# Kernel optimization log

Hardware: AMD Instinct MI355X
Metric: run time of the kernel (lower is better)

The kernel has to match this reference:

```python
import jax, jax.numpy as jnp
import numpy as np

P, M, N, H, B, E, K = 50, 512, 1024, 256, 8, 400, 5
ALPHA_MAX, TAU_MAX, RHO_MAX, ETA_MAX = 0.01, 1.0, 1.0, 1.0
LEAK = 0.01  # F.leaky_relu default slope


def _lrelu(x):
    return jnp.where(x >= 0, x, LEAK * x)


def _layernorm(x, g, b, eps=1e-5):
    mu = jnp.mean(x, axis=-1, keepdims=True)
    var = jnp.mean((x - mu) ** 2, axis=-1, keepdims=True)
    return (x - mu) * jax.lax.rsqrt(var + eps) * g + b


def setup_inputs() -> dict:
    ks = iter(jax.random.split(jax.random.key(0), 16))

    def w(fin, fout):
        return jax.random.normal(next(ks), (fin, fout), jnp.float32) * np.float32(np.sqrt(2.0 / (fin + fout)))

    H4 = 4 * H
    inp = {
        'A': jax.random.normal(next(ks), (1, P, M, N), jnp.float32) * 0.05,
        'b': jax.random.normal(next(ks), (B, P, M, 1), jnp.float32),
        'W1': w(2 * N, H), 'b1': jnp.zeros(H), 'bn1_s': jnp.ones(H), 'bn1_t': jnp.zeros(H),
        'W2': w(H, 2 * H), 'b2': jnp.zeros(2 * H), 'bn2_s': jnp.ones(2 * H), 'bn2_t': jnp.zeros(2 * H),
        'W3': w(2 * H, H4), 'b3': jnp.zeros(H4), 'bn3_s': jnp.ones(H4), 'bn3_t': jnp.zeros(H4),
        'W4': w(H4, H4), 'b4': jnp.zeros(H4), 'bn4_s': jnp.ones(H4), 'bn4_t': jnp.zeros(H4),
        'W5': w(H4, H4), 'b5': jnp.zeros(H4), 'bn5_s': jnp.ones(H4), 'bn5_t': jnp.zeros(H4),
        'ln_g': jnp.ones(H4), 'ln_b': jnp.zeros(H4),
        'Wd1': w(P * H4, H4), 'bd1': jnp.zeros(H4), 'lnd1_g': jnp.ones(H4), 'lnd1_b': jnp.zeros(H4),
        'Wd2': w(H4, 2 * H), 'bd2': jnp.zeros(2 * H), 'lnd2_g': jnp.ones(2 * H), 'lnd2_b': jnp.zeros(2 * H),
        'Wd3': w(2 * H, H), 'bd3': jnp.zeros(H), 'lnd3_g': jnp.ones(H), 'lnd3_b': jnp.zeros(H),
        'Wfc': w(H, 4) * 0.1, 'bfc': jnp.zeros(4),
        'edge_index': jax.random.randint(next(ks), (2, E), 0, P),
    }
    return inp


def reference(A, b, W1, b1, bn1_s, bn1_t, W2, b2, bn2_s, bn2_t, W3, b3, bn3_s, bn3_t,
              W4, b4, bn4_s, bn4_t, W5, b5, bn5_s, bn5_t, ln_g, ln_b,
              Wd1, bd1, lnd1_g, lnd1_b, Wd2, bd2, lnd2_g, lnd2_b, Wd3, bd3, lnd3_g, lnd3_b,
              Wfc, bfc, edge_index):
    A0 = A[0]                                             # [P,M,N]
    AtA = jnp.einsum('pmi,pmj->pij', A0, A0)              # [P,N,N]  (compute_Atx(A))
    Atb = jnp.einsum('pmn,bpm->bpn', A0, b[..., 0])[..., None]  # [B,P,N,1]

    src, dst = edge_index[0], edge_index[1]
    ones_e = jnp.ones((E,), A.dtype)
    # sum_neighbors: out-degree of each node p, shape broadcastable to [B,P,1,1]
    sum_nb = jax.ops.segment_sum(ones_e, src, num_segments=P)[None, :, None, None]

    # GCNConv normalization with self loops: norm_ij = deg_i^-1/2 * deg_j^-1/2
    sl = jnp.arange(P)
    src_a = jnp.concatenate([src, sl])
    dst_a = jnp.concatenate([dst, sl])
    deg = jax.ops.segment_sum(jnp.ones((E + P,), A.dtype), dst_a, num_segments=P)
    dinv = jax.lax.rsqrt(deg)
    coef = (dinv[src_a] * dinv[dst_a])[:, None]           # [E+P,1]

    convs = [(W1, b1, bn1_s, bn1_t), (W2, b2, bn2_s, bn2_t), (W3, b3, bn3_s, bn3_t),
             (W4, b4, bn4_s, bn4_t), (W5, b5, bn5_s, bn5_t)]

    def gconv(x, W, bias):                                # x: [P,Cin]
        xw = x @ W
        return jax.ops.segment_sum(xw[src_a] * coef, dst_a, num_segments=P) + bias

    def encode_one(feat):                                 # feat: [P,2N]
        x = feat
        for (W, bias, s, t) in convs:
            # leaky_relu -> BatchNorm1d (eval: affine scale/shift) -> dropout (eval: id)
            x = _lrelu(gconv(x, W, bias)) * s + t
        return _layernorm(x, ln_g, ln_b).reshape(-1)      # [P*4H]

    enc = jax.vmap(encode_one)

    y = jnp.zeros((B, P, N, 1), A.dtype)
    U = jnp.zeros_like(y)
    delta = jnp.zeros_like(y)
    Ys = []
    for k in range(K):
        AtAy = jnp.einsum('pij,bpj->bpi', AtA, y[..., 0])[..., None]  # [B,P,N,1]
        feat = jnp.concatenate([AtAy, Atb], axis=2)[..., 0]           # [B,P,2N]
        code = enc(feat)                                              # [B,P*4H]
        h = _lrelu(_layernorm(code @ Wd1 + bd1, lnd1_g, lnd1_b))
        h = _lrelu(_layernorm(h @ Wd2 + bd2, lnd2_g, lnd2_b))
        h = _lrelu(_layernorm(h @ Wd3 + bd3, lnd3_g, lnd3_b))
        hyp = jnp.clip(jax.nn.sigmoid(h @ Wfc + bfc), 1e-4, 0.99).reshape(B, 4, 1, 1, 1)
        alpha = hyp[:, 0] * ALPHA_MAX
        tau = hyp[:, 1] * TAU_MAX
        rho = hyp[:, 2] * RHO_MAX
        eta = hyp[:, 3] * ETA_MAX
        g = AtAy - Atb + jnp.sign(y) * tau + U * sum_nb + delta * rho
        mg = max(30.0, 100.0 - k)
        g = jnp.clip(g, -mg, mg)
        mv = max(10.0, 200.0 - k * 3)
        y = jnp.clip(y - alpha * g, -mv, mv)
        # compute_delta: for each directed edge (s,d): delta[s]+= (y_s-y_d); delta[d]-= (y_s-y_d)
        diff = y[:, src] - y[:, dst]                                  # [B,E,N,1]
        delta = jnp.zeros_like(y).at[:, src].add(diff).at[:, dst].add(-diff)
        U = jnp.clip(U + delta * eta, -mv, mv)
        Ys.append(y)
    return jnp.stack(Ys)                                              # [K,B,P,N,1]
```

## Files before the change

### kernel.cpp

```cpp
#include <hip/hip_runtime.h>

#define PP 50
#define MM 512
#define NN 1024

constexpr size_t F_ATB   = 0;
constexpr size_t F_ATAY  = F_ATB   + 409600;
constexpr size_t F_Y     = F_ATAY  + 409600;
constexpr size_t F_U     = F_Y     + 409600;
constexpr size_t F_DELTA = F_U     + 409600;
constexpr size_t F_BT    = F_DELTA + 409600;
constexpr size_t F_AYT   = F_BT    + 204800;
constexpr size_t F_Z     = F_AYT   + 204800;
constexpr size_t F_X0    = F_Z     + 917504;
constexpr size_t F_X1    = F_X0    + 409600;
constexpr size_t F_CODET = F_X1    + 409600;
constexpr size_t F_PART  = F_CODET + 409600;
constexpr size_t F_DPART = F_PART  + 3670016;
constexpr size_t F_DPART2= F_DPART + 2097152;
constexpr size_t F_H1    = F_DPART2+ 32768;
constexpr size_t F_H2    = F_H1    + 8192;
constexpr size_t F_H3    = F_H2    + 4096;
constexpr size_t F_HYP   = F_H3    + 2048;
constexpr size_t F_GCCO  = F_HYP   + 64;
constexpr size_t F_SUMNB = F_GCCO  + 512;
constexpr size_t F_END   = F_SUMNB + 64;

__device__ __forceinline__ float lrelu(float v) { return v >= 0.f ? v : 0.01f * v; }

__device__ __forceinline__ void bred2(float& s1, float& s2, float* sm) {
  #pragma unroll
  for (int off = 32; off > 0; off >>= 1) {
    s1 += __shfl_down(s1, off);
    s2 += __shfl_down(s2, off);
  }
  int w = threadIdx.x >> 6, l = threadIdx.x & 63;
  if (l == 0) { sm[w] = s1; sm[4 + w] = s2; }
  __syncthreads();
  s1 = sm[0] + sm[1] + sm[2] + sm[3];
  s2 = sm[4] + sm[5] + sm[6] + sm[7];
}

__global__ __launch_bounds__(512) void ksetup(const int* __restrict__ ei, float* sumnb,
                                              float* gccoef, int* gcoff, int* gcsrc,
                                              int* nbroff, int* nbridx) {
  __shared__ int cin[PP];
  __shared__ int cou[PP];
  __shared__ float sdinv[PP];
  __shared__ int goff[PP + 1], noff[PP + 1];
  int t = threadIdx.x;
  const int* src = ei;
  const int* dst = ei + 400;
  if (t < PP) { cin[t] = 0; cou[t] = 0; }
  __syncthreads();
  if (t < 400) {
    atomicAdd(&cou[src[t]], 1);
    atomicAdd(&cin[dst[t]], 1);
  }
  __syncthreads();
  if (t < PP) {
    sdinv[t] = rsqrtf((float)(cin[t] + 1));
    sumnb[t] = (float)cou[t];
  }
  __syncthreads();
  if (t == 0) {
    goff[0] = 0; noff[0] = 0;
    for (int p = 0; p < PP; ++p) {
      goff[p + 1] = goff[p] + cin[p] + 1;
      noff[p + 1] = noff[p] + cin[p] + cou[p];
    }
  }
  __syncthreads();
  if (t <= PP) { gcoff[t] = goff[t]; nbroff[t] = noff[t]; }
  if (t < 400) {
    int d = dst[t], s = src[t];
    int slot = 0;
    for (int e = 0; e < t; ++e) slot += (dst[e] == d) ? 1 : 0;
    int pos = goff[d] + slot;
    gcsrc[pos] = s;
    gccoef[pos] = sdinv[s] * sdinv[d];
  }
  if (t < PP) {
    int pos = goff[t] + cin[t];
    gcsrc[pos] = t;
    gccoef[pos] = sdinv[t] * sdinv[t];
  }
  if (t < 400) {
    int s = src[t], d = dst[t];
    int so = 0, si = 0;
    for (int e = 0; e < t; ++e) {
      so += (src[e] == s) ? 1 : 0;
      si += (dst[e] == d) ? 1 : 0;
    }
    nbridx[noff[s] + so] = d;
    nbridx[noff[d] + cou[d] + si] = s;
  }
}

__global__ __launch_bounds__(256) void kbt(const float* __restrict__ b, float* __restrict__ bt) {
  int i = blockIdx.x * 256 + threadIdx.x;
  int bb = i / (PP * MM);
  int r = i - bb * (PP * MM);
  bt[r * 8 + bb] = b[i];
}

__global__ __launch_bounds__(256) void katz(const float* __restrict__ A, const float* __restrict__ q,
                                            float* __restrict__ outv) {
  __shared__ float red[4][64][8];
  int nb = blockIdx.x, p = blockIdx.y, t = threadIdx.x;
  int ln = t & 63, mg = t >> 6;
  int n = nb * 64 + ln;
  float acc[8] = {0, 0, 0, 0, 0, 0, 0, 0};
  const float* ap = A + ((size_t)p * MM + mg * 128) * NN + n;
  const float* qp = q + ((size_t)p * MM + mg * 128) * 8;
  for (int m0 = 0; m0 < 128; m0 += 8) {
    float av[8];
    #pragma unroll
    for (int u = 0; u < 8; ++u) av[u] = ap[(size_t)(m0 + u) * NN];
    #pragma unroll
    for (int u = 0; u < 8; ++u) {
      #pragma unroll
      for (int bb = 0; bb < 8; ++bb) acc[bb] += av[u] * qp[(m0 + u) * 8 + bb];
    }
  }
  #pragma unroll
  for (int bb = 0; bb < 8; ++bb) red[mg][ln][bb] = acc[bb];
  __syncthreads();
  if (mg == 0) {
    #pragma unroll
    for (int bb = 0; bb < 8; ++bb) {
      float v = red[0][ln][bb] + red[1][ln][bb] + red[2][ln][bb] + red[3][ln][bb];
      outv[((size_t)bb * PP + p) * NN + n] = v;
    }
  }
}

__global__ __launch_bounds__(256) void kay(const float* __restrict__ A, const float* __restrict__ y,
                                           float* __restrict__ ayt) {
  __shared__ __align__(16) float sy[8][NN];
  int p = blockIdx.x, mb = blockIdx.y, t = threadIdx.x;
  #pragma unroll
  for (int bb = 0; bb < 8; ++bb)
    for (int n = t; n < NN; n += 256) sy[bb][n] = y[(bb * PP + p) * NN + n];
  __syncthreads();
  int w = t >> 6, l = t & 63;
  int mbase = mb * 64 + w * 16;
  for (int i = 0; i < 8; ++i) {
    int m0 = mbase + 2 * i, m1 = m0 + 1;
    float acc0[8] = {0, 0, 0, 0, 0, 0, 0, 0};
    float acc1[8] = {0, 0, 0, 0, 0, 0, 0, 0};
    const float* a0p = A + ((size_t)p * MM + m0) * NN;
    const float* a1p = a0p + NN;
    #pragma unroll
    for (int jj = 0; jj < 4; ++jj) {
      int n0 = 4 * l + 256 * jj;
      float4 a0 = *(const float4*)(a0p + n0);
      float4 a1 = *(const float4*)(a1p + n0);
      #pragma unroll
      for (int bb = 0; bb < 8; ++bb) {
        float4 yv = *(const float4*)&sy[bb][n0];
        acc0[bb] += a0.x * yv.x + a0.y * yv.y + a0.z * yv.z + a0.w * yv.w;
        acc1[bb] += a1.x * yv.x + a1.y * yv.y + a1.z * yv.z + a1.w * yv.w;
      }
    }
    #pragma unroll
    for (int off = 32; off > 0; off >>= 1) {
      #pragma unroll
      for (int bb = 0; bb < 8; ++bb) {
        acc0[bb] += __shfl_down(acc0[bb], off);
        acc1[bb] += __shfl_down(acc1[bb], off);
      }
    }
    if (l == 0) {
      #pragma unroll
      for (int bb = 0; bb < 8; ++bb) {
        ayt[((size_t)p * MM + m0) * 8 + bb] = acc0[bb];
        ayt[((size_t)p * MM + m1) * 8 + bb] = acc1[bb];
      }
    }
  }
}

__global__ __launch_bounds__(256) void kgather1(const float* __restrict__ atay,
                                                const float* __restrict__ atb,
                                                float* __restrict__ z,
                                                const int* __restrict__ gcoff,
                                                const int* __restrict__ gcsrc,
                                                const float* __restrict__ gccoef, int first) {
  int r = blockIdx.x, cc = blockIdx.y, t = threadIdx.x;
  size_t zi = (size_t)r * 2048 + (size_t)cc * 256 + t;
  if (r >= 400) { z[zi] = 0.f; return; }
  int srcA = (cc < 4) ? 1 : 0;
  if (srcA && first) { z[zi] = 0.f; return; }
  int b = r / 50, p = r - b * 50;
  int c = (srcA ? cc * 256 : (cc - 4) * 256) + t;
  const float* src = srcA ? atay : atb;
  float acc = 0.f;
  int o0 = gcoff[p], o1 = gcoff[p + 1];
  for (int idx = o0; idx < o1; ++idx)
    acc += gccoef[idx] * src[((size_t)b * 50 + gcsrc[idx]) * 1024 + c];
  z[zi] = acc;
}

__global__ __launch_bounds__(256) void kgatherX(const float* __restrict__ x, float* __restrict__ z,
                                                int Cin, const int* __restrict__ gcoff,
                                                const int* __restrict__ gcsrc,
                                                const float* __restrict__ gccoef) {
  int r = blockIdx.x, cc = blockIdx.y, t = threadIdx.x;
  int c = cc * 256 + t;
  size_t zi = (size_t)r * Cin + c;
  if (r >= 400) { z[zi] = 0.f; return; }
  int b = r / 50, p = r - b * 50;
  float acc = 0.f;
  int o0 = gcoff[p], o1 = gcoff[p + 1];
  for (int idx = o0; idx < o1; ++idx)
    acc += gccoef[idx] * x[((size_t)b * 50 + gcsrc[idx]) * Cin + c];
  z[zi] = acc;
}

__global__ __launch_bounds__(256) void kgemm(const float* __restrict__ X, const float* __restrict__ W,
                                             float* __restrict__ part, int K, int C, int krange) {
  int cb = blockIdx.x, rb = blockIdx.y, s = blockIdx.z;
  int t = threadIdx.x;
  __shared__ __align__(16) float As[16][64];
  __shared__ __align__(16) float Bs[16][68];
  int rbase = rb * 64, cbase = cb * 64;
  int k0 = s * krange, kend = k0 + krange;
  float acc[4][4] = {};
  int tx = t & 15, ty = t >> 4;
  int lrow = t >> 2, lk = (t & 3) * 4;
  int brow = t >> 4, bc = (t & 15) * 4;
  for (int k = k0; k < kend; k += 16) {
    float4 av = *(const float4*)(X + (size_t)(rbase + lrow) * K + k + lk);
    As[lk + 0][lrow] = av.x;
    As[lk + 1][lrow] = av.y;
    As[lk + 2][lrow] = av.z;
    As[lk + 3][lrow] = av.w;
    *(float4*)&Bs[brow][bc] = *(const float4*)(W + (size_t)(k + brow) * C + cbase + bc);
    __syncthreads();
    #pragma unroll
    for (int kk = 0; kk < 16; ++kk) {
      float4 a = *(const float4*)&As[kk][ty * 4];
      float4 b = *(const float4*)&Bs[kk][tx * 4];
      float aa[4] = {a.x, a.y, a.z, a.w};
      float bb[4] = {b.x, b.y, b.z, b.w};
      #pragma unroll
      for (int i = 0; i < 4; ++i)
        #pragma unroll
        for (int j = 0; j < 4; ++j) acc[i][j] += aa[i] * bb[j];
    }
    __syncthreads();
  }
  #pragma unroll
  for (int i = 0; i < 4; ++i) {
    int r = rbase + ty * 4 + i;
    *(float4*)&part[((size_t)s * 448 + r) * C + cbase + tx * 4] =
        make_float4(acc[i][0], acc[i][1], acc[i][2], acc[i][3]);
  }
}

template <int NCH, bool LASTLN>
__global__ __launch_bounds__(256) void kredE(const float* __restrict__ part, int S,
                                             const float* __restrict__ bias,
                                             const float* __restrict__ bns,
                                             const float* __restrict__ bnt,
                                             float* __restrict__ xout,
                                             const float* __restrict__ lng,
                                             const float* __restrict__ lnb,
                                             float* __restrict__ codet) {
  __shared__ float smr[8];
  constexpr int C = NCH * 256;
  int r = blockIdx.x, t = threadIdx.x;
  float vals[NCH];
  #pragma unroll
  for (int ch = 0; ch < NCH; ++ch) {
    int c = ch * 256 + t;
    float acc = 0.f;
    const float* pp = part + (size_t)r * C + c;
    #pragma unroll 4
    for (int s = 0; s < S; ++s) acc += pp[(size_t)s * 448 * C];
    float v = lrelu(acc + bias[c]);
    vals[ch] = v * bns[c] + bnt[c];
  }
  if (!LASTLN) {
    #pragma unroll
    for (int ch = 0; ch < NCH; ++ch)
      xout[(size_t)r * C + ch * 256 + t] = vals[ch];
  } else {
    float s1 = 0.f, s2 = 0.f;
    #pragma unroll
    for (int ch = 0; ch < NCH; ++ch) { s1 += vals[ch]; s2 += vals[ch] * vals[ch]; }
    bred2(s1, s2, smr);
    float mu = s1 / (float)C;
    float var = s2 / (float)C - mu * mu;
    float rs = rsqrtf(var + 1e-5f);
    int b = r / 50, p = r - b * 50;
    #pragma unroll
    for (int ch = 0; ch < NCH; ++ch) {
      int c = ch * 256 + t;
      codet[((size_t)p * C + c) * 8 + b] = (vals[ch] - mu) * rs * lng[c] + lnb[c];
    }
  }
}

__global__ __launch_bounds__(256) void kwd1(const float* __restrict__ W,
                                            const float* __restrict__ in_t,
                                            float* __restrict__ dpart) {
  int t = threadIdx.x, s = blockIdx.x;
  int k0 = s * 200;
  float4 acc[8];
  #pragma unroll
  for (int b = 0; b < 8; ++b) acc[b] = make_float4(0.f, 0.f, 0.f, 0.f);
  const float* wp = W + (size_t)k0 * 1024 + 4 * t;
  const float* qp = in_t + (size_t)k0 * 8;
  for (int k = 0; k < 200; k += 4) {
    float4 wv[4], qa[4], qb[4];
    #pragma unroll
    for (int u = 0; u < 4; ++u) {
      wv[u] = *(const float4*)(wp + (size_t)(k + u) * 1024);
      qa[u] = *(const float4*)(qp + (k + u) * 8);
      qb[u] = *(const float4*)(qp + (k + u) * 8 + 4);
    }
    #pragma unroll
    for (int u = 0; u < 4; ++u) {
      float qs[8] = {qa[u].x, qa[u].y, qa[u].z, qa[u].w, qb[u].x, qb[u].y, qb[u].z, qb[u].w};
      #pragma unroll
      for (int b = 0; b < 8; ++b) {
        acc[b].x += wv[u].x * qs[b];
        acc[b].y += wv[u].y * qs[b];
        acc[b].z += wv[u].z * qs[b];
        acc[b].w += wv[u].w * qs[b];
      }
    }
  }
  #pragma unroll
  for (int b = 0; b < 8; ++b)
    *(float4*)&dpart[(size_t)(s * 8 + b) * 1024 + 4 * t] = acc[b];
}

__global__ __launch_bounds__(256) void kredA(const float* __restrict__ dpart,
                                             float* __restrict__ dpart2) {
  int cb = blockIdx.x, sg = blockIdx.y, b = blockIdx.z, t = threadIdx.x;
  int c = cb * 256 + t;
  float acc = 0.f;
  const float* pp = dpart + ((size_t)(sg * 64) * 8 + b) * 1024 + c;
  #pragma unroll 8
  for (int i = 0; i < 64; ++i) acc += pp[(size_t)i * 8 * 1024];
  dpart2[((size_t)sg * 8 + b) * 1024 + c] = acc;
}

__global__ __launch_bounds__(128) void kwdS(const float* __restrict__ W,
                                            const float* __restrict__ in_t,
                                            float* __restrict__ part, int C, int krange) {
  int t = threadIdx.x, s = blockIdx.x;
  int k0 = s * krange;
  float4 acc[8];
  #pragma unroll
  for (int b = 0; b < 8; ++b) acc[b] = make_float4(0.f, 0.f, 0.f, 0.f);
  const float* wp = W + (size_t)k0 * C + 4 * t;
  const float* qp = in_t + (size_t)k0 * 8;
  for (int k = 0; k < krange; ++k) {
    float4 wv = *(const float4*)(wp + (size_t)k * C);
    float4 qa = *(const float4*)(qp + k * 8);
    float4 qb = *(const float4*)(qp + k * 8 + 4);
    float qs[8] = {qa.x, qa.y, qa.z, qa.w, qb.x, qb.y, qb.z, qb.w};
    #pragma unroll
    for (int b = 0; b < 8; ++b) {
      acc[b].x += wv.x * qs[b];
      acc[b].y += wv.y * qs[b];
      acc[b].z += wv.z * qs[b];
      acc[b].w += wv.w * qs[b];
    }
  }
  #pragma unroll
  for (int b = 0; b < 8; ++b)
    *(float4*)&part[(size_t)(s * 8 + b) * C + 4 * t] = acc[b];
}

__global__ __launch_bounds__(1024) void kred(const float* __restrict__ part, int S, int C,
                                             const float* __restrict__ bias,
                                             const float* __restrict__ g,
                                             const float* __restrict__ be,
                                             float* __restrict__ out_t) {
  __shared__ float sm[32];
  int b = blockIdx.x, t = threadIdx.x;
  float v = bias[t];
  const float* pp = part + (size_t)b * C + t;
  #pragma unroll 4
  for (int s = 0; s < S; ++s) v += pp[(size_t)s * 8 * C];
  float s1 = v, s2 = v * v;
  #pragma unroll
  for (int off = 32; off > 0; off >>= 1) {
    s1 += __shfl_down(s1, off);
    s2 += __shfl_down(s2, off);
  }
  int w = t >> 6, l = t & 63;
  int nw = blockDim.x >> 6;
  if (l == 0) { sm[w] = s1; sm[16 + w] = s2; }
  __syncthreads();
  s1 = 0.f; s2 = 0.f;
  for (int i = 0; i < nw; ++i) { s1 += sm[i]; s2 += sm[16 + i]; }
  float inv = 1.f / (float)C;
  float mu = s1 * inv;
  float var = s2 * inv - mu * mu;
  float rs = rsqrtf(var + 1e-5f);
  float o = lrelu((v - mu) * rs * g[t] + be[t]);
  out_t[t * 8 + b] = o;
}

__global__ __launch_bounds__(256) void kwfc(const float* __restrict__ Wfc, const float* __restrict__ bfc,
                                            const float* __restrict__ h3t, float* __restrict__ hyp) {
  __shared__ float sd[32][257];
  int t = threadIdx.x;
  float4 w = *(const float4*)(Wfc + t * 4);
  #pragma unroll
  for (int bb = 0; bb < 8; ++bb) {
    float x = h3t[t * 8 + bb];
    sd[bb * 4 + 0][t] = x * w.x;
    sd[bb * 4 + 1][t] = x * w.y;
    sd[bb * 4 + 2][t] = x * w.z;
    sd[bb * 4 + 3][t] = x * w.w;
  }
  __syncthreads();
  if (t < 32) {
    float s = 0.f;
    for (int i = 0; i < 256; ++i) s += sd[t][i];
    s += bfc[t & 3];
    float sig = 1.f / (1.f + expf(-s));
    sig = fminf(fmaxf(sig, 1e-4f), 0.99f);
    hyp[t] = sig;
  }
}

__global__ __launch_bounds__(256) void kyupd(const float* __restrict__ atay, const float* __restrict__ atb,
                                             float* y, const float* __restrict__ U,
                                             const float* __restrict__ delta,
                                             const float* __restrict__ hyp,
                                             const float* __restrict__ sumnb, float* __restrict__ outp,
                                             float mg, float mv, int first) {
  int i = blockIdx.x * 256 + threadIdx.x;
  int bb = i / (PP * NN);
  int rem = i - bb * (PP * NN);
  int p = rem >> 10;
  float alpha = hyp[bb * 4 + 0] * 0.01f;
  float g;
  float yv;
  if (first) {
    yv = 0.f;
    g = -atb[i];
  } else {
    float tau = hyp[bb * 4 + 1];
    float rho = hyp[bb * 4 + 2];
    yv = y[i];
    float sg = (yv > 0.f) ? 1.f : ((yv < 0.f) ? -1.f : 0.f);
    g = atay[i] - atb[i] + sg * tau + U[i] * sumnb[p] + delta[i] * rho;
  }
  g = fminf(fmaxf(g, -mg), mg);
  float yn = yv - alpha * g;
  yn = fminf(fmaxf(yn, -mv), mv);
  y[i] = yn;
  outp[i] = yn;
}

__global__ __launch_bounds__(256) void kdeltaU(const float* __restrict__ y, float* __restrict__ delta,
                                               float* __restrict__ U, const float* __restrict__ hyp,
                                               const int* __restrict__ nbroff,
                                               const int* __restrict__ nbridx, float mv, int first) {
  int t = threadIdx.x;
  int n = blockIdx.x * 256 + t;
  int p = blockIdx.y;
  int bb = blockIdx.z;
  int o0 = nbroff[p], o1 = nbroff[p + 1];
  int base = bb * (PP * NN) + p * NN;
  float d = (float)(o1 - o0) * y[base + n];
  for (int idx = o0; idx < o1; ++idx) {
    int q = nbridx[idx];
    d -= y[bb * (PP * NN) + q * NN + n];
  }
  delta[base + n] = d;
  float eta = hyp[bb * 4 + 3];
  float u0 = first ? 0.f : U[base + n];
  float u = u0 + d * eta;
  U[base + n] = fminf(fmaxf(u, -mv), mv);
}

extern "C" void kernel_launch(void* const* d_in, const int* in_sizes, int n_in,
                              void* d_out, int out_size, void* d_ws, size_t ws_size,
                              hipStream_t stream) {
  const float* A    = (const float*)d_in[0];
  const float* bvec = (const float*)d_in[1];
  const float* W1 = (const float*)d_in[2];
  const float* b1 = (const float*)d_in[3];
  const float* bn1s = (const float*)d_in[4];
  const float* bn1t = (const float*)d_in[5];
  const float* W2 = (const float*)d_in[6];
  const float* b2 = (const float*)d_in[7];
  const float* bn2s = (const float*)d_in[8];
  const float* bn2t = (const float*)d_in[9];
  const float* W3 = (const float*)d_in[10];
  const float* b3 = (const float*)d_in[11];
  const float* bn3s = (const float*)d_in[12];
  const float* bn3t = (const float*)d_in[13];
  const float* W4 = (const float*)d_in[14];
  const float* b4 = (const float*)d_in[15];
  const float* bn4s = (const float*)d_in[16];
  const float* bn4t = (const float*)d_in[17];
  const float* W5 = (const float*)d_in[18];
  const float* b5 = (const float*)d_in[19];
  const float* bn5s = (const float*)d_in[20];
  const float* bn5t = (const float*)d_in[21];
  const float* lng = (const float*)d_in[22];
  const float* lnb = (const float*)d_in[23];
  const float* Wd1 = (const float*)d_in[24];
  const float* bd1 = (const float*)d_in[25];
  const float* lnd1g = (const float*)d_in[26];
  const float* lnd1b = (const float*)d_in[27];
  const float* Wd2 = (const float*)d_in[28];
  const float* bd2 = (const float*)d_in[29];
  const float* lnd2g = (const float*)d_in[30];
  const float* lnd2b = (const float*)d_in[31];
  const float* Wd3 = (const float*)d_in[32];
  const float* bd3 = (const float*)d_in[33];
  const float* lnd3g = (const float*)d_in[34];
  const float* lnd3b = (const float*)d_in[35];
  const float* Wfc = (const float*)d_in[36];
  const float* bfc = (const float*)d_in[37];
  const int* ei = (const int*)d_in[38];

  float* out = (float*)d_out;
  float* wsf = (float*)d_ws;
  float* atb = wsf + F_ATB;
  float* atay = wsf + F_ATAY;
  float* yb = wsf + F_Y;
  float* Ub = wsf + F_U;
  float* db = wsf + F_DELTA;
  float* bt = wsf + F_BT;
  float* ayt = wsf + F_AYT;
  float* z = wsf + F_Z;
  float* x0 = wsf + F_X0;
  float* x1 = wsf + F_X1;
  float* codet = wsf + F_CODET;
  float* part = wsf + F_PART;
  float* dpart = wsf + F_DPART;
  float* dpart2 = wsf + F_DPART2;
  float* h1t = wsf + F_H1;
  float* h2t = wsf + F_H2;
  float* h3t = wsf + F_H3;
  float* hyp = wsf + F_HYP;
  float* gccoef = wsf + F_GCCO;
  float* sumnb = wsf + F_SUMNB;
  int* wsi = (int*)(wsf + F_END);
  int* gcoff = wsi;
  int* gcsrc = wsi + 64;
  int* nbroff = wsi + 576;
  int* nbridx = wsi + 640;

  ksetup<<<1, 512, 0, stream>>>(ei, sumnb, gccoef, gcoff, gcsrc, nbroff, nbridx);
  kbt<<<800, 256, 0, stream>>>(bvec, bt);
  katz<<<dim3(16, 50), 256, 0, stream>>>(A, bt, atb);

  const float mgs[5] = {100.f, 99.f, 98.f, 97.f, 96.f};
  const float mvs[5] = {200.f, 197.f, 194.f, 191.f, 188.f};

  for (int k = 0; k < 5; ++k) {
    if (k > 0) {
      kay<<<dim3(50, 8), 256, 0, stream>>>(A, yb, ayt);
      katz<<<dim3(16, 50), 256, 0, stream>>>(A, ayt, atay);
    }
    kgather1<<<dim3(448, 8), 256, 0, stream>>>(atay, atb, z, gcoff, gcsrc, gccoef, k == 0);
    kgemm<<<dim3(4, 7, 16), 256, 0, stream>>>(z, W1, part, 2048, 256, 128);
    kredE<1, false><<<400, 256, 0, stream>>>(part, 16, b1, bn1s, bn1t, x0, nullptr, nullptr, nullptr);
    kgatherX<<<dim3(448, 1), 256, 0, stream>>>(x0, z, 256, gcoff, gcsrc, gccoef);
    kgemm<<<dim3(8, 7, 8), 256, 0, stream>>>(z, W2, part, 256, 512, 32);
    kredE<2, false><<<400, 256, 0, stream>>>(part, 8, b2, bn2s, bn2t, x1, nullptr, nullptr, nullptr);
    kgatherX<<<dim3(448, 2), 256, 0, stream>>>(x1, z, 512, gcoff, gcsrc, gccoef);
    kgemm<<<dim3(16, 7, 8), 256, 0, stream>>>(z, W3, part, 512, 1024, 64);
    kredE<4, false><<<400, 256, 0, stream>>>(part, 8, b3, bn3s, bn3t, x0, nullptr, nullptr, nullptr);
    kgatherX<<<dim3(448, 4), 256, 0, stream>>>(x0, z, 1024, gcoff, gcsrc, gccoef);
    kgemm<<<dim3(16, 7, 8), 256, 0, stream>>>(z, W4, part, 1024, 1024, 128);
    kredE<4, false><<<400, 256, 0, stream>>>(part, 8, b4, bn4s, bn4t, x1, nullptr, nullptr, nullptr);
    kgatherX<<<dim3(448, 4), 256, 0, stream>>>(x1, z, 1024, gcoff, gcsrc, gccoef);
    kgemm<<<dim3(16, 7, 8), 256, 0, stream>>>(z, W5, part, 1024, 1024, 128);
    kredE<4, true><<<400, 256, 0, stream>>>(part, 8, b5, bn5s, bn5t, nullptr, lng, lnb, codet);
    kwd1<<<256, 256, 0, stream>>>(Wd1, codet, dpart);
    kredA<<<dim3(4, 4, 8), 256, 0, stream>>>(dpart, dpart2);
    kred<<<8, 1024, 0, stream>>>(dpart2, 4, 1024, bd1, lnd1g, lnd1b, h1t);
    kwdS<<<64, 128, 0, stream>>>(Wd2, h1t, dpart, 512, 16);
    kred<<<8, 512, 0, stream>>>(dpart, 64, 512, bd2, lnd2g, lnd2b, h2t);
    kwdS<<<32, 64, 0, stream>>>(Wd3, h2t, dpart, 256, 16);
    kred<<<8, 256, 0, stream>>>(dpart, 32, 256, bd3, lnd3g, lnd3b, h3t);
    kwfc<<<1, 256, 0, stream>>>(Wfc, bfc, h3t, hyp);
    kyupd<<<1600, 256, 0, stream>>>(atay, atb, yb, Ub, db, hyp, sumnb,
                                    out + (size_t)k * 409600, mgs[k], mvs[k], k == 0);
    kdeltaU<<<dim3(4, 50, 8), 256, 0, stream>>>(yb, db, Ub, hyp, nbroff, nbridx, mvs[k], k == 0);
  }
}
```

Baseline: 1.568 ms.

## Reorder graph-conv as GEMM-then-gather, widen GEMM tiles, restructure kay and kwd1

Each graph-conv layer used to gather neighbour features first and then run the GEMM. It now runs the GEMM on the raw features and fuses the gather into the bias/BN epilogue, using linearity (G·X)·W = G·(X·W). This drops the separate gather kernels and the padded z buffer. For k==0 the first GEMM reads only the atb half of the input, because atay is zero there. The GEMM tile widens to 64x128 and a separate split-K reduce kernel is added. kay is remapped so each lane handles one batch and a 128-column chunk. kwd1 is restructured to drop its second reduction kernel. The cost is an extra kernel launch per layer for the split-K reduce and different floating-point summation order.

```diff
diff --git a/kernel.cpp b/kernel.cpp
--- a/kernel.cpp
+++ b/kernel.cpp
@@ -11,14 +11,12 @@
 constexpr size_t F_DELTA = F_U     + 409600;
 constexpr size_t F_BT    = F_DELTA + 409600;
 constexpr size_t F_AYT   = F_BT    + 204800;
-constexpr size_t F_Z     = F_AYT   + 204800;
-constexpr size_t F_X0    = F_Z     + 917504;
-constexpr size_t F_X1    = F_X0    + 409600;
-constexpr size_t F_CODET = F_X1    + 409600;
+constexpr size_t F_X0    = F_AYT   + 204800;
+constexpr size_t F_X1    = F_X0    + 458752;
+constexpr size_t F_XW    = F_X1    + 458752;
+constexpr size_t F_CODET = F_XW    + 458752;
 constexpr size_t F_PART  = F_CODET + 409600;
-constexpr size_t F_DPART = F_PART  + 3670016;
-constexpr size_t F_DPART2= F_DPART + 2097152;
-constexpr size_t F_H1    = F_DPART2+ 32768;
+constexpr size_t F_H1    = F_PART  + 3670016;
 constexpr size_t F_H2    = F_H1    + 8192;
 constexpr size_t F_H3    = F_H2    + 4096;
 constexpr size_t F_HYP   = F_H3    + 2048;
@@ -139,146 +137,133 @@
                                            float* __restrict__ ayt) {
   __shared__ __align__(16) float sy[8][NN];
   int p = blockIdx.x, mb = blockIdx.y, t = threadIdx.x;
-  #pragma unroll
-  for (int bb = 0; bb < 8; ++bb)
-    for (int n = t; n < NN; n += 256) sy[bb][n] = y[(bb * PP + p) * NN + n];
+  for (int idx = t; idx < 8 * NN; idx += 256) {
+    int bb = idx >> 10, n = idx & 1023;
+    sy[bb][n] = y[((size_t)bb * PP + p) * NN + n];
+  }
   __syncthreads();
   int w = t >> 6, l = t & 63;
-  int mbase = mb * 64 + w * 16;
-  for (int i = 0; i < 8; ++i) {
-    int m0 = mbase + 2 * i, m1 = m0 + 1;
-    float acc0[8] = {0, 0, 0, 0, 0, 0, 0, 0};
-    float acc1[8] = {0, 0, 0, 0, 0, 0, 0, 0};
-    const float* a0p = A + ((size_t)p * MM + m0) * NN;
-    const float* a1p = a0p + NN;
-    #pragma unroll
-    for (int jj = 0; jj < 4; ++jj) {
-      int n0 = 4 * l + 256 * jj;
-      float4 a0 = *(const float4*)(a0p + n0);
-      float4 a1 = *(const float4*)(a1p + n0);
+  int b = l & 7, nc = l >> 3;
+  int n0 = nc * 128;
+  for (int i = 0; i < 4; ++i) {
+    int m0 = mb * 64 + w * 16 + i * 4;
+    float acc[4] = {0.f, 0.f, 0.f, 0.f};
+    const float* ap = A + ((size_t)p * MM + m0) * NN + n0;
+    #pragma unroll 8
+    for (int j = 0; j < 32; ++j) {
+      float4 yv = *(const float4*)&sy[b][n0 + 4 * j];
       #pragma unroll
-      for (int bb = 0; bb < 8; ++bb) {
-        float4 yv = *(const float4*)&sy[bb][n0];
-        acc0[bb] += a0.x * yv.x + a0.y * yv.y + a0.z * yv.z + a0.w * yv.w;
-        acc1[bb] += a1.x * yv.x + a1.y * yv.y + a1.z * yv.z + a1.w * yv.w;
+      for (int mm = 0; mm < 4; ++mm) {
+        float4 av = *(const float4*)(ap + (size_t)mm * NN + 4 * j);
+        acc[mm] += av.x * yv.x + av.y * yv.y + av.z * yv.z + av.w * yv.w;
       }
     }
     #pragma unroll
-    for (int off = 32; off > 0; off >>= 1) {
+    for (int mm = 0; mm < 4; ++mm) {
+      acc[mm] += __shfl_xor(acc[mm], 8);
+      acc[mm] += __shfl_xor(acc[mm], 16);
+      acc[mm] += __shfl_xor(acc[mm], 32);
+    }
+    if (nc == 0) {
       #pragma unroll
-      for (int bb = 0; bb < 8; ++bb) {
-        acc0[bb] += __shfl_down(acc0[bb], off);
-        acc1[bb] += __shfl_down(acc1[bb], off);
-      }
-    }
-    if (l == 0) {
-      #pragma unroll
-      for (int bb = 0; bb < 8; ++bb) {
-        ayt[((size_t)p * MM + m0) * 8 + bb] = acc0[bb];
-        ayt[((size_t)p * MM + m1) * 8 + bb] = acc1[bb];
-      }
-    }
-  }
-}
-
-__global__ __launch_bounds__(256) void kgather1(const float* __restrict__ atay,
-                                                const float* __restrict__ atb,
-                                                float* __restrict__ z,
-                                                const int* __restrict__ gcoff,
-                                                const int* __restrict__ gcsrc,
-                                                const float* __restrict__ gccoef, int first) {
-  int r = blockIdx.x, cc = blockIdx.y, t = threadIdx.x;
-  size_t zi = (size_t)r * 2048 + (size_t)cc * 256 + t;
-  if (r >= 400) { z[zi] = 0.f; return; }
-  int srcA = (cc < 4) ? 1 : 0;
-  if (srcA && first) { z[zi] = 0.f; return; }
-  int b = r / 50, p = r - b * 50;
-  int c = (srcA ? cc * 256 : (cc - 4) * 256) + t;
-  const float* src = srcA ? atay : atb;
-  float acc = 0.f;
-  int o0 = gcoff[p], o1 = gcoff[p + 1];
-  for (int idx = o0; idx < o1; ++idx)
-    acc += gccoef[idx] * src[((size_t)b * 50 + gcsrc[idx]) * 1024 + c];
-  z[zi] = acc;
-}
-
-__global__ __launch_bounds__(256) void kgatherX(const float* __restrict__ x, float* __restrict__ z,
-                                                int Cin, const int* __restrict__ gcoff,
-                                                const int* __restrict__ gcsrc,
-                                                const float* __restrict__ gccoef) {
-  int r = blockIdx.x, cc = blockIdx.y, t = threadIdx.x;
-  int c = cc * 256 + t;
-  size_t zi = (size_t)r * Cin + c;
-  if (r >= 400) { z[zi] = 0.f; return; }
-  int b = r / 50, p = r - b * 50;
-  float acc = 0.f;
-  int o0 = gcoff[p], o1 = gcoff[p + 1];
-  for (int idx = o0; idx < o1; ++idx)
-    acc += gccoef[idx] * x[((size_t)b * 50 + gcsrc[idx]) * Cin + c];
-  z[zi] = acc;
-}
-
-__global__ __launch_bounds__(256) void kgemm(const float* __restrict__ X, const float* __restrict__ W,
-                                             float* __restrict__ part, int K, int C, int krange) {
+      for (int mm = 0; mm < 4; ++mm)
+        ayt[(size_t)((size_t)p * MM + m0 + mm) * 8 + b] = acc[mm];
+    }
+  }
+}
+
+__global__ __launch_bounds__(256) void kgemm(const float* __restrict__ X, const float* __restrict__ X2,
+                                             const float* __restrict__ W, float* __restrict__ part,
+                                             int K, int C, int krange, int koff) {
+  __shared__ __align__(16) float As[16][64];
+  __shared__ __align__(16) float Bs[16][132];
   int cb = blockIdx.x, rb = blockIdx.y, s = blockIdx.z;
   int t = threadIdx.x;
-  __shared__ __align__(16) float As[16][64];
-  __shared__ __align__(16) float Bs[16][68];
-  int rbase = rb * 64, cbase = cb * 64;
-  int k0 = s * krange, kend = k0 + krange;
-  float acc[4][4] = {};
+  int rbase = rb * 64, cbase = cb * 128;
   int tx = t & 15, ty = t >> 4;
   int lrow = t >> 2, lk = (t & 3) * 4;
-  int brow = t >> 4, bc = (t & 15) * 4;
-  for (int k = k0; k < kend; k += 16) {
-    float4 av = *(const float4*)(X + (size_t)(rbase + lrow) * K + k + lk);
+  int brow = t >> 4, bc = (t & 15) * 8;
+  int k0 = koff + s * krange;
+  float acc[4][8];
+  #pragma unroll
+  for (int i = 0; i < 4; ++i)
+    #pragma unroll
+    for (int j = 0; j < 8; ++j) acc[i][j] = 0.f;
+  for (int kt = k0; kt < k0 + krange; kt += 16) {
+    int r = rbase + lrow;
+    const float* xp;
+    if (X2) {
+      xp = (kt < 1024) ? (X + (size_t)r * 1024 + kt) : (X2 + (size_t)r * 1024 + (kt - 1024));
+    } else {
+      xp = X + (size_t)r * K + kt;
+    }
+    float4 av = *(const float4*)(xp + lk);
     As[lk + 0][lrow] = av.x;
     As[lk + 1][lrow] = av.y;
     As[lk + 2][lrow] = av.z;
     As[lk + 3][lrow] = av.w;
-    *(float4*)&Bs[brow][bc] = *(const float4*)(W + (size_t)(k + brow) * C + cbase + bc);
+    const float* wp = W + (size_t)(kt + brow) * C + cbase + bc;
+    *(float4*)&Bs[brow][bc] = *(const float4*)wp;
+    *(float4*)&Bs[brow][bc + 4] = *(const float4*)(wp + 4);
     __syncthreads();
     #pragma unroll
     for (int kk = 0; kk < 16; ++kk) {
       float4 a = *(const float4*)&As[kk][ty * 4];
-      float4 b = *(const float4*)&Bs[kk][tx * 4];
-      float aa[4] = {a.x, a.y, a.z, a.w};
-      float bb[4] = {b.x, b.y, b.z, b.w};
+      float4 b0 = *(const float4*)&Bs[kk][tx * 4];
+      float4 b1 = *(const float4*)&Bs[kk][64 + tx * 4];
+      float ar[4] = {a.x, a.y, a.z, a.w};
+      float bv[8] = {b0.x, b0.y, b0.z, b0.w, b1.x, b1.y, b1.z, b1.w};
       #pragma unroll
       for (int i = 0; i < 4; ++i)
         #pragma unroll
-        for (int j = 0; j < 4; ++j) acc[i][j] += aa[i] * bb[j];
+        for (int j = 0; j < 8; ++j) acc[i][j] += ar[i] * bv[j];
     }
     __syncthreads();
   }
   #pragma unroll
   for (int i = 0; i < 4; ++i) {
     int r = rbase + ty * 4 + i;
-    *(float4*)&part[((size_t)s * 448 + r) * C + cbase + tx * 4] =
-        make_float4(acc[i][0], acc[i][1], acc[i][2], acc[i][3]);
-  }
+    float* pp = part + ((size_t)s * 448 + r) * C + cbase;
+    *(float4*)(pp + tx * 4) = make_float4(acc[i][0], acc[i][1], acc[i][2], acc[i][3]);
+    *(float4*)(pp + 64 + tx * 4) = make_float4(acc[i][4], acc[i][5], acc[i][6], acc[i][7]);
+  }
+}
+
+__global__ __launch_bounds__(256) void kredEp(const float* __restrict__ part, int S, int C,
+                                              float* __restrict__ xw) {
+  int r = blockIdx.x;
+  int c = blockIdx.y * 256 + threadIdx.x;
+  const float* pp = part + (size_t)r * C + c;
+  float acc = 0.f;
+  #pragma unroll 8
+  for (int s = 0; s < S; ++s) acc += pp[(size_t)s * 448 * C];
+  xw[(size_t)r * C + c] = acc;
 }
 
 template <int NCH, bool LASTLN>
-__global__ __launch_bounds__(256) void kredE(const float* __restrict__ part, int S,
-                                             const float* __restrict__ bias,
-                                             const float* __restrict__ bns,
-                                             const float* __restrict__ bnt,
-                                             float* __restrict__ xout,
-                                             const float* __restrict__ lng,
-                                             const float* __restrict__ lnb,
-                                             float* __restrict__ codet) {
+__global__ __launch_bounds__(256) void kgatherE(const float* __restrict__ xw,
+                                                const float* __restrict__ bias,
+                                                const float* __restrict__ bns,
+                                                const float* __restrict__ bnt,
+                                                float* __restrict__ xout,
+                                                const int* __restrict__ gcoff,
+                                                const int* __restrict__ gcsrc,
+                                                const float* __restrict__ gccoef,
+                                                const float* __restrict__ lng,
+                                                const float* __restrict__ lnb,
+                                                float* __restrict__ codet) {
   __shared__ float smr[8];
   constexpr int C = NCH * 256;
   int r = blockIdx.x, t = threadIdx.x;
+  int b = r / 50, p = r - b * 50;
+  int o0 = gcoff[p], o1 = gcoff[p + 1];
   float vals[NCH];
   #pragma unroll
   for (int ch = 0; ch < NCH; ++ch) {
     int c = ch * 256 + t;
     float acc = 0.f;
-    const float* pp = part + (size_t)r * C + c;
-    #pragma unroll 4
-    for (int s = 0; s < S; ++s) acc += pp[(size_t)s * 448 * C];
+    for (int idx = o0; idx < o1; ++idx)
+      acc += gccoef[idx] * xw[((size_t)b * 50 + gcsrc[idx]) * C + c];
     float v = lrelu(acc + bias[c]);
     vals[ch] = v * bns[c] + bnt[c];
   }
@@ -294,7 +279,6 @@
     float mu = s1 / (float)C;
     float var = s2 / (float)C - mu * mu;
     float rs = rsqrtf(var + 1e-5f);
-    int b = r / 50, p = r - b * 50;
     #pragma unroll
     for (int ch = 0; ch < NCH; ++ch) {
       int c = ch * 256 + t;
@@ -306,47 +290,29 @@
 __global__ __launch_bounds__(256) void kwd1(const float* __restrict__ W,
                                             const float* __restrict__ in_t,
                                             float* __restrict__ dpart) {
-  int t = threadIdx.x, s = blockIdx.x;
-  int k0 = s * 200;
-  float4 acc[8];
-  #pragma unroll
-  for (int b = 0; b < 8; ++b) acc[b] = make_float4(0.f, 0.f, 0.f, 0.f);
-  const float* wp = W + (size_t)k0 * 1024 + 4 * t;
+  int t = threadIdx.x, cb = blockIdx.x, s = blockIdx.y;
+  int c = cb * 256 + t;
+  int k0 = s * 800;
+  float acc[8] = {0, 0, 0, 0, 0, 0, 0, 0};
+  const float* wp = W + (size_t)k0 * 1024 + c;
   const float* qp = in_t + (size_t)k0 * 8;
-  for (int k = 0; k < 200; k += 4) {
-    float4 wv[4], qa[4], qb[4];
-    #pragma unroll
-    for (int u = 0; u < 4; ++u) {
-      wv[u] = *(const float4*)(wp + (size_t)(k + u) * 1024);
-      qa[u] = *(const float4*)(qp + (k + u) * 8);
-      qb[u] = *(const float4*)(qp + (k + u) * 8 + 4);
-    }
-    #pragma unroll
-    for (int u = 0; u < 4; ++u) {
-      float qs[8] = {qa[u].x, qa[u].y, qa[u].z, qa[u].w, qb[u].x, qb[u].y, qb[u].z, qb[u].w};
-      #pragma unroll
-      for (int b = 0; b < 8; ++b) {
-        acc[b].x += wv[u].x * qs[b];
-        acc[b].y += wv[u].y * qs[b];
-        acc[b].z += wv[u].z * qs[b];
-        acc[b].w += wv[u].w * qs[b];
-      }
+  for (int k = 0; k < 800; k += 16) {
+    float wv[16];
+    #pragma unroll
+    for (int u = 0; u < 16; ++u) wv[u] = wp[(size_t)(k + u) * 1024];
+    #pragma unroll
+    for (int u = 0; u < 16; ++u) {
+      float4 qa = *(const float4*)(qp + (k + u) * 8);
+      float4 qb = *(const float4*)(qp + (k + u) * 8 + 4);
+      acc[0] += wv[u] * qa.x; acc[1] += wv[u] * qa.y;
+      acc[2] += wv[u] * qa.z; acc[3] += wv[u] * qa.w;
+      acc[4] += wv[u] * qb.x; acc[5] += wv[u] * qb.y;
+      acc[6] += wv[u] * qb.z; acc[7] += wv[u] * qb.w;
     }
   }
   #pragma unroll
   for (int b = 0; b < 8; ++b)
-    *(float4*)&dpart[(size_t)(s * 8 + b) * 1024 + 4 * t] = acc[b];
-}
-
-__global__ __launch_bounds__(256) void kredA(const float* __restrict__ dpart,
-                                             float* __restrict__ dpart2) {
-  int cb = blockIdx.x, sg = blockIdx.y, b = blockIdx.z, t = threadIdx.x;
-  int c = cb * 256 + t;
-  float acc = 0.f;
-  const float* pp = dpart + ((size_t)(sg * 64) * 8 + b) * 1024 + c;
-  #pragma unroll 8
-  for (int i = 0; i < 64; ++i) acc += pp[(size_t)i * 8 * 1024];
-  dpart2[((size_t)sg * 8 + b) * 1024 + c] = acc;
+    dpart[(size_t)(s * 8 + b) * 1024 + c] = acc[b];
 }
 
 __global__ __launch_bounds__(128) void kwdS(const float* __restrict__ W,
@@ -386,7 +352,7 @@
   int b = blockIdx.x, t = threadIdx.x;
   float v = bias[t];
   const float* pp = part + (size_t)b * C + t;
-  #pragma unroll 4
+  #pragma unroll 8
   for (int s = 0; s < S; ++s) v += pp[(size_t)s * 8 * C];
   float s1 = v, s2 = v * v;
   #pragma unroll
@@ -443,8 +409,7 @@
   int rem = i - bb * (PP * NN);
   int p = rem >> 10;
   float alpha = hyp[bb * 4 + 0] * 0.01f;
-  float g;
-  float yv;
+  float g, yv;
   if (first) {
     yv = 0.f;
     g = -atb[i];
@@ -536,13 +501,12 @@
   float* db = wsf + F_DELTA;
   float* bt = wsf + F_BT;
   float* ayt = wsf + F_AYT;
-  float* z = wsf + F_Z;
   float* x0 = wsf + F_X0;
   float* x1 = wsf + F_X1;
+  float* xw = wsf + F_XW;
   float* codet = wsf + F_CODET;
   float* part = wsf + F_PART;
-  float* dpart = wsf + F_DPART;
-  float* dpart2 = wsf + F_DPART2;
+  float* dpart = part;
   float* h1t = wsf + F_H1;
   float* h2t = wsf + F_H2;
   float* h3t = wsf + F_H3;
@@ -567,24 +531,33 @@
       kay<<<dim3(50, 8), 256, 0, stream>>>(A, yb, ayt);
       katz<<<dim3(16, 50), 256, 0, stream>>>(A, ayt, atay);
     }
-    kgather1<<<dim3(448, 8), 256, 0, stream>>>(atay, atb, z, gcoff, gcsrc, gccoef, k == 0);
-    kgemm<<<dim3(4, 7, 16), 256, 0, stream>>>(z, W1, part, 2048, 256, 128);
-    kredE<1, false><<<400, 256, 0, stream>>>(part, 16, b1, bn1s, bn1t, x0, nullptr, nullptr, nullptr);
-    kgatherX<<<dim3(448, 1), 256, 0, stream>>>(x0, z, 256, gcoff, gcsrc, gccoef);
-    kgemm<<<dim3(8, 7, 8), 256, 0, stream>>>(z, W2, part, 256, 512, 32);
-    kredE<2, false><<<400, 256, 0, stream>>>(part, 8, b2, bn2s, bn2t, x1, nullptr, nullptr, nullptr);
-    kgatherX<<<dim3(448, 2), 256, 0, stream>>>(x1, z, 512, gcoff, gcsrc, gccoef);
-    kgemm<<<dim3(16, 7, 8), 256, 0, stream>>>(z, W3, part, 512, 1024, 64);
-    kredE<4, false><<<400, 256, 0, stream>>>(part, 8, b3, bn3s, bn3t, x0, nullptr, nullptr, nullptr);
-    kgatherX<<<dim3(448, 4), 256, 0, stream>>>(x0, z, 1024, gcoff, gcsrc, gccoef);
-    kgemm<<<dim3(16, 7, 8), 256, 0, stream>>>(z, W4, part, 1024, 1024, 128);
-    kredE<4, false><<<400, 256, 0, stream>>>(part, 8, b4, bn4s, bn4t, x1, nullptr, nullptr, nullptr);
-    kgatherX<<<dim3(448, 4), 256, 0, stream>>>(x1, z, 1024, gcoff, gcsrc, gccoef);
-    kgemm<<<dim3(16, 7, 8), 256, 0, stream>>>(z, W5, part, 1024, 1024, 128);
-    kredE<4, true><<<400, 256, 0, stream>>>(part, 8, b5, bn5s, bn5t, nullptr, lng, lnb, codet);
-    kwd1<<<256, 256, 0, stream>>>(Wd1, codet, dpart);
-    kredA<<<dim3(4, 4, 8), 256, 0, stream>>>(dpart, dpart2);
-    kred<<<8, 1024, 0, stream>>>(dpart2, 4, 1024, bd1, lnd1g, lnd1b, h1t);
+    if (k == 0) {
+      kgemm<<<dim3(2, 7, 8), 256, 0, stream>>>(atay, atb, W1, part, 1024, 256, 128, 1024);
+      kredEp<<<dim3(400, 1), 256, 0, stream>>>(part, 8, 256, xw);
+    } else {
+      kgemm<<<dim3(2, 7, 16), 256, 0, stream>>>(atay, atb, W1, part, 1024, 256, 128, 0);
+      kredEp<<<dim3(400, 1), 256, 0, stream>>>(part, 16, 256, xw);
+    }
+    kgatherE<1, false><<<400, 256, 0, stream>>>(xw, b1, bn1s, bn1t, x0, gcoff, gcsrc, gccoef,
+                                                nullptr, nullptr, nullptr);
+    kgemm<<<dim3(4, 7, 8), 256, 0, stream>>>(x0, nullptr, W2, part, 256, 512, 32, 0);
+    kredEp<<<dim3(400, 2), 256, 0, stream>>>(part, 8, 512, xw);
+    kgatherE<2, false><<<400, 256, 0, stream>>>(xw, b2, bn2s, bn2t, x1, gcoff, gcsrc, gccoef,
+                                                nullptr, nullptr, nullptr);
+    kgemm<<<dim3(8, 7, 8), 256, 0, stream>>>(x1, nullptr, W3, part, 512, 1024, 64, 0);
+    kredEp<<<dim3(400, 4), 256, 0, stream>>>(part, 8, 1024, xw);
+    kgatherE<4, false><<<400, 256, 0, stream>>>(xw, b3, bn3s, bn3t, x0, gcoff, gcsrc, gccoef,
+                                                nullptr, nullptr, nullptr);
+    kgemm<<<dim3(8, 7, 8), 256, 0, stream>>>(x0, nullptr, W4, part, 1024, 1024, 128, 0);
+    kredEp<<<dim3(400, 4), 256, 0, stream>>>(part, 8, 1024, xw);
+    kgatherE<4, false><<<400, 256, 0, stream>>>(xw, b4, bn4s, bn4t, x1, gcoff, gcsrc, gccoef,
+                                                nullptr, nullptr, nullptr);
+    kgemm<<<dim3(8, 7, 8), 256, 0, stream>>>(x1, nullptr, W5, part, 1024, 1024, 128, 0);
+    kredEp<<<dim3(400, 4), 256, 0, stream>>>(part, 8, 1024, xw);
+    kgatherE<4, true><<<400, 256, 0, stream>>>(xw, b5, bn5s, bn5t, nullptr, gcoff, gcsrc, gccoef,
+                                               lng, lnb, codet);
+    kwd1<<<dim3(4, 64), 256, 0, stream>>>(Wd1, codet, dpart);
+    kred<<<8, 1024, 0, stream>>>(dpart, 64, 1024, bd1, lnd1g, lnd1b, h1t);
     kwdS<<<64, 128, 0, stream>>>(Wd2, h1t, dpart, 512, 16);
     kred<<<8, 512, 0, stream>>>(dpart, 64, 512, bd2, lnd2g, lnd2b, h2t);
     kwdS<<<32, 64, 0, stream>>>(Wd3, h2t, dpart, 256, 16);
```

After: 1.852 ms. 1.18x slower.
